# Kernel tuning notes

Measured on AMD Instinct MI355X. Metric: run time of the kernel, lower is better.

## Reference

```python
import jax, jax.numpy as jnp
import numpy as np

D = 1024
H = 16
DH = D // H


def setup_inputs() -> dict:
    key = jax.random.key(0)
    ks = jax.random.split(key, 9)
    s = 1.0 / np.sqrt(D)
    return {
        "x": jax.random.normal(ks[0], (4, 2048, D), dtype=jnp.float32),
        "wq": jax.random.uniform(ks[1], (D, D), jnp.float32, -s, s),
        "bq": jax.random.uniform(ks[2], (D,), jnp.float32, -s, s),
        "wk": jax.random.uniform(ks[3], (D, D), jnp.float32, -s, s),
        "bk": jax.random.uniform(ks[4], (D,), jnp.float32, -s, s),
        "wv": jax.random.uniform(ks[5], (D, D), jnp.float32, -s, s),
        "bv": jax.random.uniform(ks[6], (D,), jnp.float32, -s, s),
        "wo": jax.random.uniform(ks[7], (D, D), jnp.float32, -s, s),
        "bo": jax.random.uniform(ks[8], (D,), jnp.float32, -s, s),
    }


def reference(x, wq, bq, wk, bk, wv, bv, wo, bo):
    B, S, _ = x.shape
    # projections + split heads: [B, S, D] -> [B, H, S, Dh]
    def split(t):
        return t.reshape(B, S, H, DH).transpose(0, 2, 1, 3)
    q = split(x @ wq + bq)
    k = split(x @ wk + bk)
    v = split(x @ wv + bv)
    scale = 1.0 / jnp.sqrt(jnp.float32(DH))
    scores = jnp.einsum("bhqd,bhkd->bhqk", q, k) * scale  # [B,H,S,S]
    att = jax.nn.softmax(scores, axis=-1)
    out = jnp.einsum("bhqk,bhkd->bhqd", att, v)  # [B,H,S,Dh]
    out = out.transpose(0, 2, 1, 3).reshape(B, S, D)
    return out @ wo + bo
```

## Files before the change

kernel.cpp:

```cpp
#include <hip/hip_runtime.h>
#include <stdint.h>

typedef float f32x4 __attribute__((ext_vector_type(4)));
typedef __bf16 bf16x8 __attribute__((ext_vector_type(8)));
typedef unsigned short ushort_t;
typedef ushort_t ushortx8 __attribute__((ext_vector_type(8)));
typedef ushort_t ushortx4 __attribute__((ext_vector_type(4)));

#define DEV static __device__ __forceinline__

DEV ushort_t f2bf(float f) {
  union { float f; uint32_t u; } v; v.f = f;
  uint32_t u = v.u;
  return (ushort_t)((u + 0x7FFFu + ((u >> 16) & 1u)) >> 16);
}

DEV uint32_t pkbf(float a, float b) {
  __bf16 x = (__bf16)a, y = (__bf16)b;
  return (uint32_t)__builtin_bit_cast(unsigned short, x) |
         ((uint32_t)__builtin_bit_cast(unsigned short, y) << 16);
}

DEV void cp16(const void* g, void* l) {
  __builtin_amdgcn_global_load_lds((const __attribute__((address_space(1))) unsigned int*)g,
                                   (__attribute__((address_space(3))) unsigned int*)l,
                                   16, 0, 0);
}

DEV f32x4 mfma16(bf16x8 a, bf16x8 b, f32x4 c) {
  return __builtin_amdgcn_mfma_f32_16x16x32_bf16(a, b, c, 0, 0, 0);
}

__global__ __launch_bounds__(256) void k_prep(
    const float* __restrict__ x, ushort_t* __restrict__ xb,
    const float* __restrict__ wq, const float* __restrict__ wk,
    const float* __restrict__ wv, const float* __restrict__ wo,
    ushort_t* __restrict__ wqkvT, ushort_t* __restrict__ woT) {
  __shared__ float tile[32][33];
  int b = blockIdx.x;
  if (b < 4096) {
    size_t idx = ((size_t)b * 256 + threadIdx.x) * 8;
    const float4* src = (const float4*)(x + idx);
    float4 a = src[0], c = src[1];
    ushortx8 o;
    o[0] = f2bf(a.x); o[1] = f2bf(a.y); o[2] = f2bf(a.z); o[3] = f2bf(a.w);
    o[4] = f2bf(c.x); o[5] = f2bf(c.y); o[6] = f2bf(c.z); o[7] = f2bf(c.w);
    *(ushortx8*)(xb + idx) = o;
  } else {
    int t = b - 4096;
    int which = t >> 10;
    const float* src = (which == 0) ? wq : (which == 1) ? wk : (which == 2) ? wv : wo;
    ushort_t* dst = (which == 0) ? wqkvT
                    : (which == 1) ? wqkvT + 1024 * 1024
                    : (which == 2) ? wqkvT + 2 * 1024 * 1024
                                   : woT;
    int tt = t & 1023;
    int c0 = (tt & 31) * 32, r0 = (tt >> 5) * 32;
    int tx = threadIdx.x & 31, ty = threadIdx.x >> 5;
#pragma unroll
    for (int i = ty; i < 32; i += 8)
      tile[i][tx] = src[(size_t)(r0 + i) * 1024 + c0 + tx];
    __syncthreads();
#pragma unroll
    for (int i = ty; i < 32; i += 8)
      dst[(size_t)(c0 + i) * 1024 + r0 + tx] = f2bf(tile[tx][i]);
  }
}

__global__ __launch_bounds__(256) void k_transpose_v(const ushort_t* __restrict__ vw,
                                                     ushort_t* __restrict__ vtw) {
  __shared__ ushort_t t[64][72];
  int tid = threadIdx.x;
  int bh = blockIdx.y, s0 = blockIdx.x * 64;
#pragma unroll
  for (int n = 0; n < 2; ++n) {
    int row = (tid >> 3) + n * 32, ch = (tid & 7) * 8;
    *(ushortx8*)&t[row][ch] =
        *(const ushortx8*)&vw[((size_t)bh * 2048 + s0 + row) * 64 + ch];
  }
  __syncthreads();
#pragma unroll
  for (int n = 0; n < 2; ++n) {
    int dh = (tid >> 3) + n * 32, sc = (tid & 7) * 8;
    ushortx8 o;
#pragma unroll
    for (int k = 0; k < 8; ++k) o[k] = t[sc + k][dh];
    *(ushortx8*)&vtw[((size_t)bh * 64 + dh) * 2048 + s0 + sc] = o;
  }
}

template <int MODE>
__global__ __launch_bounds__(256, 2) void k_gemm(
    const ushort_t* __restrict__ A, const ushort_t* __restrict__ Bt,
    const float* __restrict__ b0, const float* __restrict__ b1,
    const float* __restrict__ b2, ushort_t* __restrict__ qw,
    ushort_t* __restrict__ kw, ushort_t* __restrict__ vw,
    float* __restrict__ outf) {
  const int K = 1024;
  __shared__ ushort_t As[128 * 32];
  __shared__ ushort_t Bs[128 * 32];
  int tid = threadIdx.x;
  int w = tid >> 6, lane = tid & 63, l16 = lane & 15, lg = lane >> 4;
  int m0 = blockIdx.x * 128, n0 = blockIdx.y * 128;
  int wm = (w >> 1) * 64, wn = (w & 1) * 64;
  f32x4 acc[4][4] = {};

  const ushort_t* Ag = A + (size_t)(m0 + (tid >> 2)) * K + (tid & 3) * 8;
  const ushort_t* Bg = Bt + (size_t)(n0 + (tid >> 2)) * K + (tid & 3) * 8;

  for (int k0 = 0; k0 < K; k0 += 32) {
    cp16(Ag + k0, As + w * 512);
    cp16(Ag + k0 + 64 * K, As + 2048 + w * 512);
    cp16(Bg + k0, Bs + w * 512);
    cp16(Bg + k0 + 64 * K, Bs + 2048 + w * 512);
    __syncthreads();
    bf16x8 af[4], bfr[4];
#pragma unroll
    for (int i = 0; i < 4; ++i)
      af[i] = *(const bf16x8*)&As[(wm + i * 16 + l16) * 32 + lg * 8];
#pragma unroll
    for (int j = 0; j < 4; ++j)
      bfr[j] = *(const bf16x8*)&Bs[(wn + j * 16 + l16) * 32 + lg * 8];
#pragma unroll
    for (int i = 0; i < 4; ++i)
#pragma unroll
      for (int j = 0; j < 4; ++j)
        acc[i][j] = mfma16(af[i], bfr[j], acc[i][j]);
    __syncthreads();
  }

  if (MODE == 0) {
    const float QSCALE = 0.18033688011112042f;
    int p = m0 >> 10;
    const float* bias = (p == 0) ? b0 : (p == 1) ? b1 : b2;
    ushort_t* dst = (p == 0) ? qw : (p == 1) ? kw : vw;
    float qs = (p == 0) ? QSCALE : 1.0f;
    int cbase = m0 & 1023;
#pragma unroll
    for (int i = 0; i < 4; ++i) {
      int oc = cbase + wm + i * 16 + lg * 4;
      int h = oc >> 6, dh0 = oc & 63;
      float4 bb = *(const float4*)&bias[oc];
#pragma unroll
      for (int j = 0; j < 4; ++j) {
        int tok = n0 + wn + j * 16 + l16;
        size_t base =
            ((size_t)((tok >> 11) * 16 + h) * 2048 + (tok & 2047)) * 64 + dh0;
        ushortx4 pk;
        pk[0] = f2bf((acc[i][j][0] + bb.x) * qs);
        pk[1] = f2bf((acc[i][j][1] + bb.y) * qs);
        pk[2] = f2bf((acc[i][j][2] + bb.z) * qs);
        pk[3] = f2bf((acc[i][j][3] + bb.w) * qs);
        *(ushortx4*)&dst[base] = pk;
      }
    }
  } else {
#pragma unroll
    for (int j = 0; j < 4; ++j) {
      int col = n0 + wn + j * 16 + l16;
      float bb = b0[col];
#pragma unroll
      for (int i = 0; i < 4; ++i) {
#pragma unroll
        for (int r = 0; r < 4; ++r) {
          int row = m0 + wm + i * 16 + lg * 4 + r;
          outf[(size_t)row * 1024 + col] = acc[i][j][r] + bb;
        }
      }
    }
  }
}

__global__ __launch_bounds__(512, 4) void k_attn(
    const ushort_t* __restrict__ qg, const ushort_t* __restrict__ kg,
    const ushort_t* __restrict__ vtg, ushort_t* __restrict__ att) {
  __shared__ ushort_t Ks[128 * 64];
  __shared__ ushort_t Vs[64 * 128];
  __shared__ ushort_t Ps[8][16 * 128];
  int tid = threadIdx.x;
  int w = tid >> 6, lane = tid & 63, l16 = lane & 15, lg = lane >> 4;
  int i = blockIdx.x;
  int bh = (i & 7) * 8 + ((i >> 3) & 7);
  int q0 = (i >> 6) * 256;
  const ushort_t* qh = qg + (size_t)bh * 2048 * 64;

  const ushort_t* kstage = kg + (size_t)bh * 2048 * 64 + (size_t)(tid >> 3) * 64 +
                           (size_t)(((tid & 7) ^ ((tid >> 3) & 7)) * 8);
  const ushort_t* vstage = vtg + (size_t)bh * 64 * 2048 + (size_t)(tid >> 4) * 2048 +
                           (size_t)(((tid & 15) ^ ((tid >> 4) & 15)) * 8);

  bf16x8 qf[2][2];
#pragma unroll
  for (int st = 0; st < 2; ++st)
#pragma unroll
    for (int ks = 0; ks < 2; ++ks)
      qf[st][ks] = *(const bf16x8*)(qh + (size_t)(q0 + w * 32 + st * 16 + l16) * 64 +
                                    ks * 32 + lg * 8);

  bf16x8 vone;
#pragma unroll
  for (int t = 0; t < 8; ++t) vone[t] = (__bf16)1.0f;

  f32x4 o[2][5] = {};

  for (int kb = 0; kb < 2048; kb += 128) {
    __syncthreads();
    cp16(kstage + (size_t)kb * 64, Ks + w * 512);
    cp16(kstage + (size_t)(kb + 64) * 64, Ks + 4096 + w * 512);
    cp16(vstage + kb, Vs + w * 512);
    cp16(vstage + kb + (size_t)32 * 2048, Vs + 4096 + w * 512);
    __syncthreads();

#pragma unroll
    for (int hf = 0; hf < 2; ++hf) {
      f32x4 sc[2][4] = {};
#pragma unroll
      for (int jt = 0; jt < 4; ++jt) {
        int row = hf * 64 + jt * 16 + l16;
        bf16x8 kf0 = *(const bf16x8*)&Ks[row * 64 + ((lg) ^ (l16 & 7)) * 8];
        bf16x8 kf1 = *(const bf16x8*)&Ks[row * 64 + ((lg + 4) ^ (l16 & 7)) * 8];
        sc[0][jt] = mfma16(kf0, qf[0][0], sc[0][jt]);
        sc[0][jt] = mfma16(kf1, qf[0][1], sc[0][jt]);
        sc[1][jt] = mfma16(kf0, qf[1][0], sc[1][jt]);
        sc[1][jt] = mfma16(kf1, qf[1][1], sc[1][jt]);
      }
#pragma unroll
      for (int st = 0; st < 2; ++st)
#pragma unroll
        for (int jt = 0; jt < 4; ++jt) {
          float e0 = __builtin_amdgcn_exp2f(sc[st][jt][0]);
          float e1 = __builtin_amdgcn_exp2f(sc[st][jt][1]);
          float e2 = __builtin_amdgcn_exp2f(sc[st][jt][2]);
          float e3 = __builtin_amdgcn_exp2f(sc[st][jt][3]);
          uint32_t* dst =
              (uint32_t*)&Ps[w][l16 * 128 +
                                (((st * 8 + jt * 2 + (lg >> 1)) ^ l16) * 8) +
                                (lg & 1) * 4];
          dst[0] = pkbf(e0, e1);
          dst[1] = pkbf(e2, e3);
        }
#pragma unroll
      for (int ks = 0; ks < 2; ++ks) {
        int kk = hf * 2 + ks;
        bf16x8 pf0 =
            *(const bf16x8*)&Ps[w][l16 * 128 + (((ks * 4 + lg) ^ l16) * 8)];
        bf16x8 pf1 =
            *(const bf16x8*)&Ps[w][l16 * 128 + (((8 + ks * 4 + lg) ^ l16) * 8)];
        o[0][4] = mfma16(pf0, vone, o[0][4]);
        o[1][4] = mfma16(pf1, vone, o[1][4]);
#pragma unroll
        for (int dt = 0; dt < 4; ++dt) {
          int vrow = dt * 16 + l16;
          bf16x8 vf =
              *(const bf16x8*)&Vs[vrow * 128 + (((kk * 4 + lg) ^ l16) * 8)];
          o[0][dt] = mfma16(pf0, vf, o[0][dt]);
          o[1][dt] = mfma16(pf1, vf, o[1][dt]);
        }
      }
    }
  }

  int bi = bh >> 4, h = bh & 15;
#pragma unroll
  for (int st = 0; st < 2; ++st) {
    f32x4 inv;
#pragma unroll
    for (int r = 0; r < 4; ++r) inv[r] = __builtin_amdgcn_rcpf(o[st][4][r]);
#pragma unroll
    for (int dt = 0; dt < 4; ++dt)
#pragma unroll
      for (int r = 0; r < 4; ++r) {
        int srow = q0 + w * 32 + st * 16 + lg * 4 + r;
        int col = h * 64 + dt * 16 + l16;
        att[(size_t)(bi * 2048 + srow) * 1024 + col] = f2bf(o[st][dt][r] * inv[r]);
      }
  }
}

extern "C" void kernel_launch(void* const* d_in, const int* in_sizes, int n_in,
                              void* d_out, int out_size, void* d_ws, size_t ws_size,
                              hipStream_t stream) {
  const float* x = (const float*)d_in[0];
  const float* wq = (const float*)d_in[1];
  const float* bq = (const float*)d_in[2];
  const float* wk = (const float*)d_in[3];
  const float* bk = (const float*)d_in[4];
  const float* wv = (const float*)d_in[5];
  const float* bv = (const float*)d_in[6];
  const float* wo = (const float*)d_in[7];
  const float* bo = (const float*)d_in[8];
  float* out = (float*)d_out;

  char* ws = (char*)d_ws;
  ushort_t* xb = (ushort_t*)(ws);
  ushort_t* wqkvT = (ushort_t*)(ws + 16777216);
  ushort_t* woT = (ushort_t*)(ws + 23068672);
  ushort_t* qw = (ushort_t*)(ws + 25165824);
  ushort_t* kw = (ushort_t*)(ws + 41943040);
  ushort_t* vtw = (ushort_t*)(ws + 58720256);
  ushort_t* att = (ushort_t*)(ws + 75497472);
  ushort_t* vw = att;

  k_prep<<<dim3(8192), dim3(256), 0, stream>>>(x, xb, wq, wk, wv, wo, wqkvT, woT);

  k_gemm<0><<<dim3(24, 64), dim3(256), 0, stream>>>(
      wqkvT, xb, bq, bk, bv, qw, kw, vw, nullptr);

  k_transpose_v<<<dim3(32, 64), dim3(256), 0, stream>>>(vw, vtw);

  k_attn<<<dim3(512), dim3(512), 0, stream>>>(qw, kw, vtw, att);

  k_gemm<1><<<dim3(64, 8), dim3(256), 0, stream>>>(
      att, woT, bo, nullptr, nullptr, nullptr, nullptr, nullptr, out);
}
```

Measured before the change: 294.0 us.

## Pipeline GEMMs with triple-buffered 128x256 tiles and double-buffer attention K/V

The GEMM kernel moves to 512 threads and 128x256 tiles with K-step 64. It uses a three-stage asynchronous global-to-LDS pipeline with XOR-swizzled rows, waitcnt-based barriers, and raised wave priority around the MFMA blocks. The attention kernel now processes 64-key blocks with double-buffered K/V staging, so the next block's load overlaps compute on the current one, and it drops one of the two syncthreads per iteration. These changes aim to hide memory latency and cut barrier overhead, at the cost of much larger dynamic LDS (one GEMM block per CU) and lower attention occupancy.

```diff
diff --git a/kernel.cpp b/kernel.cpp
--- a/kernel.cpp
+++ b/kernel.cpp
@@ -90,60 +90,101 @@
 }
 
 template <int MODE>
-__global__ __launch_bounds__(256, 2) void k_gemm(
+__global__ __launch_bounds__(512, 1) void k_gemm2(
     const ushort_t* __restrict__ A, const ushort_t* __restrict__ Bt,
     const float* __restrict__ b0, const float* __restrict__ b1,
     const float* __restrict__ b2, ushort_t* __restrict__ qw,
     ushort_t* __restrict__ kw, ushort_t* __restrict__ vw,
     float* __restrict__ outf) {
-  const int K = 1024;
-  __shared__ ushort_t As[128 * 32];
-  __shared__ ushort_t Bs[128 * 32];
+  extern __shared__ ushort_t lds[];
+  ushort_t* As3 = lds;
+  ushort_t* Bs3 = lds + 3 * 8192;
+  const int K = 1024, NT = 16;
   int tid = threadIdx.x;
   int w = tid >> 6, lane = tid & 63, l16 = lane & 15, lg = lane >> 4;
-  int m0 = blockIdx.x * 128, n0 = blockIdx.y * 128;
-  int wm = (w >> 1) * 64, wn = (w & 1) * 64;
+  int wr = w >> 2, wc = w & 3;
+  int m0 = blockIdx.x * 128, n0 = blockIdx.y * 256;
+
+  const ushort_t* Asrc = A + (size_t)(m0 + (tid >> 3)) * K +
+                         (size_t)(((tid & 7) ^ ((tid >> 3) & 7)) * 8);
+  const ushort_t* Bsrc = Bt + (size_t)(n0 + (tid >> 3)) * K +
+                         (size_t)(((tid & 7) ^ ((tid >> 3) & 7)) * 8);
+
+#define STAGE2(tt, buf)                                                        \
+  {                                                                            \
+    cp16(Asrc + (size_t)(tt) * 64, As3 + (buf) * 8192 + w * 512);              \
+    cp16(Asrc + (size_t)(tt) * 64 + (size_t)64 * K,                            \
+         As3 + (buf) * 8192 + 4096 + w * 512);                                 \
+    cp16(Bsrc + (size_t)(tt) * 64, Bs3 + (buf) * 16384 + w * 512);             \
+    cp16(Bsrc + (size_t)(tt) * 64 + (size_t)64 * K,                            \
+         Bs3 + (buf) * 16384 + 4096 + w * 512);                                \
+    cp16(Bsrc + (size_t)(tt) * 64 + (size_t)128 * K,                           \
+         Bs3 + (buf) * 16384 + 8192 + w * 512);                                \
+    cp16(Bsrc + (size_t)(tt) * 64 + (size_t)192 * K,                           \
+         Bs3 + (buf) * 16384 + 12288 + w * 512);                               \
+  }
+
   f32x4 acc[4][4] = {};
-
-  const ushort_t* Ag = A + (size_t)(m0 + (tid >> 2)) * K + (tid & 3) * 8;
-  const ushort_t* Bg = Bt + (size_t)(n0 + (tid >> 2)) * K + (tid & 3) * 8;
-
-  for (int k0 = 0; k0 < K; k0 += 32) {
-    cp16(Ag + k0, As + w * 512);
-    cp16(Ag + k0 + 64 * K, As + 2048 + w * 512);
-    cp16(Bg + k0, Bs + w * 512);
-    cp16(Bg + k0 + 64 * K, Bs + 2048 + w * 512);
-    __syncthreads();
-    bf16x8 af[4], bfr[4];
-#pragma unroll
-    for (int i = 0; i < 4; ++i)
-      af[i] = *(const bf16x8*)&As[(wm + i * 16 + l16) * 32 + lg * 8];
-#pragma unroll
-    for (int j = 0; j < 4; ++j)
-      bfr[j] = *(const bf16x8*)&Bs[(wn + j * 16 + l16) * 32 + lg * 8];
-#pragma unroll
-    for (int i = 0; i < 4; ++i)
-#pragma unroll
-      for (int j = 0; j < 4; ++j)
-        acc[i][j] = mfma16(af[i], bfr[j], acc[i][j]);
-    __syncthreads();
-  }
+  const int aRow = wr * 64 + l16, bRow = wc * 64 + l16, rsw = l16 & 7;
+
+  STAGE2(0, 0);
+  STAGE2(1, 1);
+  asm volatile("s_waitcnt vmcnt(6)" ::: "memory");
+  __builtin_amdgcn_s_barrier();
+
+  int qb = 0;
+  for (int t = 0; t < NT; ++t) {
+    int qn = (qb + 2 >= 3) ? qb - 1 : qb + 2;
+    int tn = (t + 2 < NT) ? t + 2 : NT - 1;
+    STAGE2(tn, qn);
+
+    bf16x8 a[4][2], b[4][2];
+    const ushort_t* Ab = As3 + qb * 8192;
+    const ushort_t* Bb = Bs3 + qb * 16384;
+#pragma unroll
+    for (int i2 = 0; i2 < 4; ++i2)
+#pragma unroll
+      for (int ks = 0; ks < 2; ++ks)
+        a[i2][ks] = *(const bf16x8*)&Ab[(aRow + i2 * 16) * 64 +
+                                        (((ks << 2) | lg) ^ rsw) * 8];
+#pragma unroll
+    for (int j2 = 0; j2 < 4; ++j2)
+#pragma unroll
+      for (int ks = 0; ks < 2; ++ks)
+        b[j2][ks] = *(const bf16x8*)&Bb[(bRow + j2 * 16) * 64 +
+                                        (((ks << 2) | lg) ^ rsw) * 8];
+    asm volatile("s_waitcnt lgkmcnt(0)" ::: "memory");
+    __builtin_amdgcn_sched_barrier(0);
+    __builtin_amdgcn_s_setprio(1);
+#pragma unroll
+    for (int i2 = 0; i2 < 4; ++i2)
+#pragma unroll
+      for (int j2 = 0; j2 < 4; ++j2)
+#pragma unroll
+        for (int ks = 0; ks < 2; ++ks)
+          acc[i2][j2] = mfma16(a[i2][ks], b[j2][ks], acc[i2][j2]);
+    __builtin_amdgcn_s_setprio(0);
+    asm volatile("s_waitcnt vmcnt(6)" ::: "memory");
+    __builtin_amdgcn_s_barrier();
+    qb = (qb + 1 >= 3) ? 0 : qb + 1;
+  }
+#undef STAGE2
 
   if (MODE == 0) {
     const float QSCALE = 0.18033688011112042f;
-    int p = m0 >> 10;
+    int p = blockIdx.x >> 3;
     const float* bias = (p == 0) ? b0 : (p == 1) ? b1 : b2;
     ushort_t* dst = (p == 0) ? qw : (p == 1) ? kw : vw;
     float qs = (p == 0) ? QSCALE : 1.0f;
-    int cbase = m0 & 1023;
+    int cbase = (m0 & 1023) + wr * 64;
 #pragma unroll
     for (int i = 0; i < 4; ++i) {
-      int oc = cbase + wm + i * 16 + lg * 4;
+      int oc = cbase + i * 16 + lg * 4;
       int h = oc >> 6, dh0 = oc & 63;
       float4 bb = *(const float4*)&bias[oc];
 #pragma unroll
       for (int j = 0; j < 4; ++j) {
-        int tok = n0 + wn + j * 16 + l16;
+        int tok = n0 + wc * 64 + j * 16 + l16;
         size_t base =
             ((size_t)((tok >> 11) * 16 + h) * 2048 + (tok & 2047)) * 64 + dh0;
         ushortx4 pk;
@@ -157,13 +198,13 @@
   } else {
 #pragma unroll
     for (int j = 0; j < 4; ++j) {
-      int col = n0 + wn + j * 16 + l16;
+      int col = n0 + wc * 64 + j * 16 + l16;
       float bb = b0[col];
 #pragma unroll
       for (int i = 0; i < 4; ++i) {
 #pragma unroll
         for (int r = 0; r < 4; ++r) {
-          int row = m0 + wm + i * 16 + lg * 4 + r;
+          int row = m0 + wr * 64 + i * 16 + lg * 4 + r;
           outf[(size_t)row * 1024 + col] = acc[i][j][r] + bb;
         }
       }
@@ -171,11 +212,11 @@
   }
 }
 
-__global__ __launch_bounds__(512, 4) void k_attn(
+__global__ __launch_bounds__(512, 2) void k_attn(
     const ushort_t* __restrict__ qg, const ushort_t* __restrict__ kg,
     const ushort_t* __restrict__ vtg, ushort_t* __restrict__ att) {
-  __shared__ ushort_t Ks[128 * 64];
-  __shared__ ushort_t Vs[64 * 128];
+  __shared__ ushort_t Ks[2][64 * 64];
+  __shared__ ushort_t Vs[2][64 * 64];
   __shared__ ushort_t Ps[8][16 * 128];
   int tid = threadIdx.x;
   int w = tid >> 6, lane = tid & 63, l16 = lane & 15, lg = lane >> 4;
@@ -186,8 +227,8 @@
 
   const ushort_t* kstage = kg + (size_t)bh * 2048 * 64 + (size_t)(tid >> 3) * 64 +
                            (size_t)(((tid & 7) ^ ((tid >> 3) & 7)) * 8);
-  const ushort_t* vstage = vtg + (size_t)bh * 64 * 2048 + (size_t)(tid >> 4) * 2048 +
-                           (size_t)(((tid & 15) ^ ((tid >> 4) & 15)) * 8);
+  const ushort_t* vstage = vtg + (size_t)bh * 64 * 2048 + (size_t)(tid >> 3) * 2048 +
+                           (size_t)(((tid & 7) ^ ((tid >> 3) & 7)) * 8);
 
   bf16x8 qf[2][2];
 #pragma unroll
@@ -203,61 +244,66 @@
 
   f32x4 o[2][5] = {};
 
-  for (int kb = 0; kb < 2048; kb += 128) {
+  cp16(kstage, &Ks[0][tid * 8]);
+  cp16(vstage, &Vs[0][tid * 8]);
+  __syncthreads();
+
+  for (int t = 0; t < 32; ++t) {
+    int cur = t & 1, nxt = cur ^ 1;
+    cp16(kstage + (size_t)(t + 1) * 64 * 64, &Ks[nxt][tid * 8]);
+    cp16(vstage + (size_t)(t + 1) * 64, &Vs[nxt][tid * 8]);
+
+    f32x4 sc[2][4] = {};
+    __builtin_amdgcn_s_setprio(1);
+#pragma unroll
+    for (int jt = 0; jt < 4; ++jt) {
+      int row = jt * 16 + l16;
+      bf16x8 kf0 = *(const bf16x8*)&Ks[cur][row * 64 + ((lg) ^ (l16 & 7)) * 8];
+      bf16x8 kf1 = *(const bf16x8*)&Ks[cur][row * 64 + ((lg + 4) ^ (l16 & 7)) * 8];
+      sc[0][jt] = mfma16(kf0, qf[0][0], sc[0][jt]);
+      sc[0][jt] = mfma16(kf1, qf[0][1], sc[0][jt]);
+      sc[1][jt] = mfma16(kf0, qf[1][0], sc[1][jt]);
+      sc[1][jt] = mfma16(kf1, qf[1][1], sc[1][jt]);
+    }
+    __builtin_amdgcn_s_setprio(0);
+
+#pragma unroll
+    for (int st = 0; st < 2; ++st)
+#pragma unroll
+      for (int jt = 0; jt < 4; ++jt) {
+        float e0 = __builtin_amdgcn_exp2f(sc[st][jt][0]);
+        float e1 = __builtin_amdgcn_exp2f(sc[st][jt][1]);
+        float e2 = __builtin_amdgcn_exp2f(sc[st][jt][2]);
+        float e3 = __builtin_amdgcn_exp2f(sc[st][jt][3]);
+        uint2 pk2;
+        pk2.x = pkbf(e0, e1);
+        pk2.y = pkbf(e2, e3);
+        *(uint2*)&Ps[w][l16 * 128 +
+                        (((st * 8 + jt * 2 + (lg >> 1)) ^ l16) * 8) +
+                        (lg & 1) * 4] = pk2;
+      }
+
+    __builtin_amdgcn_s_setprio(1);
+#pragma unroll
+    for (int ks = 0; ks < 2; ++ks) {
+      bf16x8 pf0 =
+          *(const bf16x8*)&Ps[w][l16 * 128 + (((ks * 4 + lg) ^ l16) * 8)];
+      bf16x8 pf1 =
+          *(const bf16x8*)&Ps[w][l16 * 128 + (((8 + ks * 4 + lg) ^ l16) * 8)];
+      o[0][4] = mfma16(pf0, vone, o[0][4]);
+      o[1][4] = mfma16(pf1, vone, o[1][4]);
+#pragma unroll
+      for (int dt = 0; dt < 4; ++dt) {
+        int vrow = dt * 16 + l16;
+        bf16x8 vf =
+            *(const bf16x8*)&Vs[cur][vrow * 64 + (((ks * 4 + lg) ^ (l16 & 7)) * 8)];
+        o[0][dt] = mfma16(pf0, vf, o[0][dt]);
+        o[1][dt] = mfma16(pf1, vf, o[1][dt]);
+      }
+    }
+    __builtin_amdgcn_s_setprio(0);
+
     __syncthreads();
-    cp16(kstage + (size_t)kb * 64, Ks + w * 512);
-    cp16(kstage + (size_t)(kb + 64) * 64, Ks + 4096 + w * 512);
-    cp16(vstage + kb, Vs + w * 512);
-    cp16(vstage + kb + (size_t)32 * 2048, Vs + 4096 + w * 512);
-    __syncthreads();
-
-#pragma unroll
-    for (int hf = 0; hf < 2; ++hf) {
-      f32x4 sc[2][4] = {};
-#pragma unroll
-      for (int jt = 0; jt < 4; ++jt) {
-        int row = hf * 64 + jt * 16 + l16;
-        bf16x8 kf0 = *(const bf16x8*)&Ks[row * 64 + ((lg) ^ (l16 & 7)) * 8];
-        bf16x8 kf1 = *(const bf16x8*)&Ks[row * 64 + ((lg + 4) ^ (l16 & 7)) * 8];
-        sc[0][jt] = mfma16(kf0, qf[0][0], sc[0][jt]);
-        sc[0][jt] = mfma16(kf1, qf[0][1], sc[0][jt]);
-        sc[1][jt] = mfma16(kf0, qf[1][0], sc[1][jt]);
-        sc[1][jt] = mfma16(kf1, qf[1][1], sc[1][jt]);
-      }
-#pragma unroll
-      for (int st = 0; st < 2; ++st)
-#pragma unroll
-        for (int jt = 0; jt < 4; ++jt) {
-          float e0 = __builtin_amdgcn_exp2f(sc[st][jt][0]);
-          float e1 = __builtin_amdgcn_exp2f(sc[st][jt][1]);
-          float e2 = __builtin_amdgcn_exp2f(sc[st][jt][2]);
-          float e3 = __builtin_amdgcn_exp2f(sc[st][jt][3]);
-          uint32_t* dst =
-              (uint32_t*)&Ps[w][l16 * 128 +
-                                (((st * 8 + jt * 2 + (lg >> 1)) ^ l16) * 8) +
-                                (lg & 1) * 4];
-          dst[0] = pkbf(e0, e1);
-          dst[1] = pkbf(e2, e3);
-        }
-#pragma unroll
-      for (int ks = 0; ks < 2; ++ks) {
-        int kk = hf * 2 + ks;
-        bf16x8 pf0 =
-            *(const bf16x8*)&Ps[w][l16 * 128 + (((ks * 4 + lg) ^ l16) * 8)];
-        bf16x8 pf1 =
-            *(const bf16x8*)&Ps[w][l16 * 128 + (((8 + ks * 4 + lg) ^ l16) * 8)];
-        o[0][4] = mfma16(pf0, vone, o[0][4]);
-        o[1][4] = mfma16(pf1, vone, o[1][4]);
-#pragma unroll
-        for (int dt = 0; dt < 4; ++dt) {
-          int vrow = dt * 16 + l16;
-          bf16x8 vf =
-              *(const bf16x8*)&Vs[vrow * 128 + (((kk * 4 + lg) ^ l16) * 8)];
-          o[0][dt] = mfma16(pf0, vf, o[0][dt]);
-          o[1][dt] = mfma16(pf1, vf, o[1][dt]);
-        }
-      }
-    }
   }
 
   int bi = bh >> 4, h = bh & 15;
@@ -303,13 +349,19 @@
 
   k_prep<<<dim3(8192), dim3(256), 0, stream>>>(x, xb, wq, wk, wv, wo, wqkvT, woT);
 
-  k_gemm<0><<<dim3(24, 64), dim3(256), 0, stream>>>(
+  const int G2_LDS = 147456;
+  hipFuncSetAttribute(reinterpret_cast<const void*>(&k_gemm2<0>),
+                      hipFuncAttributeMaxDynamicSharedMemorySize, G2_LDS);
+  hipFuncSetAttribute(reinterpret_cast<const void*>(&k_gemm2<1>),
+                      hipFuncAttributeMaxDynamicSharedMemorySize, G2_LDS);
+
+  k_gemm2<0><<<dim3(24, 32), dim3(512), G2_LDS, stream>>>(
       wqkvT, xb, bq, bk, bv, qw, kw, vw, nullptr);
 
   k_transpose_v<<<dim3(32, 64), dim3(256), 0, stream>>>(vw, vtw);
 
   k_attn<<<dim3(512), dim3(512), 0, stream>>>(qw, kw, vtw, att);
 
-  k_gemm<1><<<dim3(64, 8), dim3(256), 0, stream>>>(
+  k_gemm2<1><<<dim3(64, 4), dim3(512), G2_LDS, stream>>>(
       att, woT, bo, nullptr, nullptr, nullptr, nullptr, nullptr, out);
 }
```

Measured after the change: 286.4 us. -2.6%, faster.
